# Optimization experiments

Hardware: AMD Instinct MI355X
Metric: run time of the kernel (lower is better)

The kernel has to match this reference:

```python
import jax, jax.numpy as jnp
import numpy as np

B, D, H, DH, NQ, NK = 64, 768, 8, 128, 256, 256


def _ln(x, g, b, eps=1e-5):
    m = x.mean(-1, keepdims=True)
    v = ((x - m) ** 2).mean(-1, keepdims=True)
    return (x - m) / jnp.sqrt(v + eps) * g + b


def setup_inputs() -> dict:
    key = jax.random.key(0)
    ks = jax.random.split(key, 16)
    w = lambda k, s: jax.random.normal(k, s, jnp.float32) * 0.02
    return {
        'emb_cause': jax.random.normal(ks[0], (B, D), jnp.float32),
        'emb_action': jax.random.normal(ks[1], (B, D), jnp.float32),
        'tok_cause': jax.random.normal(ks[2], (B, NK, D), jnp.float32),
        'tok_effect': jax.random.normal(ks[3], (B, NQ, D), jnp.float32),
        'fuse_ln_g': jnp.ones(2 * D), 'fuse_ln_b': jnp.zeros(2 * D),
        'fuse_w1': w(ks[4], (2 * D, D)), 'fuse_b1': jnp.zeros(D),
        'fuse_w2': w(ks[5], (D, D)), 'fuse_b2': jnp.zeros(D),
        'delta_ln_g': jnp.ones(D), 'delta_ln_b': jnp.zeros(D),
        'delta_w': w(ks[6], (D, D)), 'delta_b': jnp.zeros(D),
        'qg_w': w(ks[7], (D, H * DH)), 'qg_b': jnp.zeros(H * DH),
        'kg_w': w(ks[8], (D, H * DH)), 'kg_b': jnp.zeros(H * DH),
        'eff_ln_g': jnp.ones(D), 'eff_ln_b': jnp.zeros(D),
        'eff_w1': w(ks[9], (D, D)), 'eff_b1': jnp.zeros(D),
        'eff_w2': w(ks[10], (D, D)), 'eff_b2': jnp.zeros(D),
        'u_w': w(ks[11], (D, H * DH)),
        'v_w': w(ks[12], (D, H * DH)),
        'logit_scale': jnp.zeros(()),
    }


def reference(emb_cause, emb_action, tok_cause, tok_effect,
              fuse_ln_g, fuse_ln_b, fuse_w1, fuse_b1, fuse_w2, fuse_b2,
              delta_ln_g, delta_ln_b, delta_w, delta_b,
              qg_w, qg_b, kg_w, kg_b,
              eff_ln_g, eff_ln_b, eff_w1, eff_b1, eff_w2, eff_b2,
              u_w, v_w, logit_scale):
    # fuse: LN -> Linear -> GELU(exact) -> Linear (dropout = identity, eval)
    ctx_in = jnp.concatenate([emb_cause, emb_action], axis=-1)  # (B, 2D)
    h = jax.nn.gelu(_ln(ctx_in, fuse_ln_g, fuse_ln_b) @ fuse_w1 + fuse_b1, approximate=False)
    ctx = h @ fuse_w2 + fuse_b2  # (B, D)

    delta_e = _ln(ctx, delta_ln_g, delta_ln_b) @ delta_w + delta_b  # (B, D)
    pooled_effect = tok_effect.mean(axis=1)  # (B, D)
    e_shifted = pooled_effect + delta_e

    eh = jax.nn.gelu(_ln(ctx, eff_ln_g, eff_ln_b) @ eff_w1 + eff_b1, approximate=False)
    effect_pred = eh @ eff_w2 + eff_b2  # (B, D)

    q_gate = 1.0 + jnp.tanh(jax.nn.silu(ctx @ qg_w + qg_b)).reshape(B, H, DH)
    k_gate = 1.0 + jnp.tanh(jax.nn.silu(ctx @ kg_w + kg_b)).reshape(B, H, DH)

    # logit bias: torch code materializes (B,H,Nq,Nk,Dh); equivalent math is a
    # per-head inner product u.v (independent of q) broadcast over Nq.
    u = (e_shifted @ u_w).reshape(B, H, DH)            # (B, H, Dh)
    v = (tok_cause @ v_w).reshape(B, NK, H, DH)        # (B, Nk, H, Dh)
    bias = jnp.einsum('bhd,bkhd->bhk', u, v) / np.float32(np.sqrt(DH))
    logit_bias = jnp.exp(logit_scale) * jnp.broadcast_to(bias[:, :, None, :], (B, H, NQ, NK))

    return (q_gate, k_gate, e_shifted, delta_e, logit_bias, effect_pred)
```

## Files before the change

### kernel.cpp

```cpp
#include <hip/hip_runtime.h>
#include <math.h>

#define TPB 256

typedef float vf4 __attribute__((ext_vector_type(4)));

__device__ __forceinline__ float gelu_f(float x) {
    return 0.5f * x * (1.0f + erff(x * 0.70710678118654752f));
}
__device__ __forceinline__ float gate_f(float x) {
    float si = x / (1.0f + expf(-x));
    return 1.0f + tanhf(si);
}

template <class XL>
__device__ __forceinline__ void gemm_tile(XL xload, const float* __restrict__ W, int Wld, int cb,
                                          int k0, int kslice, float* part, int totN, int gcol, int s,
                                          float* __restrict__ xs, float* __restrict__ wt)
{
    const int t = threadIdx.x;
    const int tr4 = (t >> 4) << 2;
    const int tc4 = (t & 15) << 2;
    const int a  = t >> 5, kk = t & 31;
    const int wk = t >> 6, wc = t & 63;
    float xv[8], wv[8];
#pragma unroll
    for (int j = 0; j < 8; ++j) {
        xv[j] = xload(a + 8 * j, k0 + kk);
        wv[j] = W[(size_t)(k0 + wk + 4 * j) * Wld + cb + wc];
    }
    float acc[4][4] = {{0.f,0.f,0.f,0.f},{0.f,0.f,0.f,0.f},{0.f,0.f,0.f,0.f},{0.f,0.f,0.f,0.f}};
    for (int kc = 0; kc < kslice; kc += 32) {
#pragma unroll
        for (int j = 0; j < 8; ++j) {
            xs[kk * 68 + a + 8 * j] = xv[j];
            wt[(wk + 4 * j) * 68 + wc] = wv[j];
        }
        __syncthreads();
        int kn = kc + 32;
        if (kn < kslice) {
#pragma unroll
            for (int j = 0; j < 8; ++j) {
                xv[j] = xload(a + 8 * j, k0 + kn + kk);
                wv[j] = W[(size_t)(k0 + kn + wk + 4 * j) * Wld + cb + wc];
            }
        }
#pragma unroll
        for (int k = 0; k < 32; ++k) {
            float4 xq = *(const float4*)&xs[k * 68 + tr4];
            float4 wq = *(const float4*)&wt[k * 68 + tc4];
            acc[0][0] += xq.x * wq.x; acc[0][1] += xq.x * wq.y; acc[0][2] += xq.x * wq.z; acc[0][3] += xq.x * wq.w;
            acc[1][0] += xq.y * wq.x; acc[1][1] += xq.y * wq.y; acc[1][2] += xq.y * wq.z; acc[1][3] += xq.y * wq.w;
            acc[2][0] += xq.z * wq.x; acc[2][1] += xq.z * wq.y; acc[2][2] += xq.z * wq.z; acc[2][3] += xq.z * wq.w;
            acc[3][0] += xq.w * wq.x; acc[3][1] += xq.w * wq.y; acc[3][2] += xq.w * wq.z; acc[3][3] += xq.w * wq.w;
        }
        __syncthreads();
    }
    float* pp = part + (size_t)(s * 64 + tr4) * totN + gcol + tc4;
#pragma unroll
    for (int i = 0; i < 4; ++i)
#pragma unroll
        for (int j = 0; j < 4; ++j)
            pp[i * totN + j] = acc[i][j];
}

#define GEMM_LDS __shared__ float xs[32 * 68]; __shared__ float wt[32 * 68];

__global__ __launch_bounds__(256) void k_front(const float* __restrict__ ec, const float* __restrict__ ea,
                        float* __restrict__ stats1,
                        const float* __restrict__ tok_effect, float* __restrict__ pp)
{
    int t = threadIdx.x;
    if (blockIdx.x < 64) {
        int r = blockIdx.x;
        __shared__ float red[4];
        float v[6]; float sum = 0.f;
#pragma unroll
        for (int j = 0; j < 6; ++j) {
            int c = t + j * TPB;
            float x = (c < 768) ? ec[r * 768 + c] : ea[r * 768 + (c - 768)];
            v[j] = x; sum += x;
        }
#pragma unroll
        for (int o_ = 32; o_ > 0; o_ >>= 1) sum += __shfl_xor(sum, o_);
        if ((t & 63) == 0) red[t >> 6] = sum;
        __syncthreads();
        sum = red[0] + red[1] + red[2] + red[3];
        float mean = sum * (1.f / 1536.f);
        __syncthreads();
        float s2 = 0.f;
#pragma unroll
        for (int j = 0; j < 6; ++j) { float d = v[j] - mean; s2 += d * d; }
#pragma unroll
        for (int o_ = 32; o_ > 0; o_ >>= 1) s2 += __shfl_xor(s2, o_);
        if ((t & 63) == 0) red[t >> 6] = s2;
        __syncthreads();
        s2 = red[0] + red[1] + red[2] + red[3];
        if (t == 0) {
            stats1[2 * r]     = mean;
            stats1[2 * r + 1] = rsqrtf(s2 * (1.f / 1536.f) + 1e-5f);
        }
    } else {
        int m = blockIdx.x - 64;
        int cch = m % 3, b = (m / 3) % 64, qz = m / 192;
        int c = cch * TPB + t;
        const float* base = tok_effect + (size_t)(b * 256 + qz * 64) * 768 + c;
        float s = 0.f;
#pragma unroll 16
        for (int q = 0; q < 64; ++q) s += base[(size_t)q * 768];
        pp[(qz * 64 + b) * 768 + c] = s;
    }
}

struct G1Args {
    const float *ec, *ea, *stats1, *flg, *flb, *w1;
    float* part1;
};
__global__ __launch_bounds__(256) void k_g1(G1Args A)
{
    GEMM_LDS;
    int ct = blockIdx.x % 12, s = blockIdx.x / 12;
    auto xl = [&](int r, int k) {
        float raw = (k < 768) ? A.ec[r * 768 + k] : A.ea[r * 768 + (k - 768)];
        float m = A.stats1[2 * r], rs = A.stats1[2 * r + 1];
        return (raw - m) * rs * A.flg[k] + A.flb[k];
    };
    gemm_tile(xl, A.w1, 768, ct * 64, s * 128, 128, A.part1, 768, ct * 64, s, xs, wt);
}

__global__ __launch_bounds__(256) void k_g2(const float* __restrict__ part1, const float* __restrict__ b1,
                                            const float* __restrict__ w2, float* __restrict__ part2)
{
    GEMM_LDS;
    int ct = blockIdx.x % 12, s = blockIdx.x / 12;
    auto xl = [&](int r, int k) {
        float v = b1[k];
#pragma unroll
        for (int q = 0; q < 12; ++q) v += part1[(size_t)(q * 64 + r) * 768 + k];
        return gelu_f(v);
    };
    gemm_tile(xl, w2, 768, ct * 64, s * 64, 64, part2, 768, ct * 64, s, xs, wt);
}

__global__ __launch_bounds__(256) void k_ln(const float* __restrict__ part2, const float* __restrict__ b2,
                                            float* __restrict__ ctx, float* __restrict__ stats2)
{
    int r = blockIdx.x, t = threadIdx.x;
    __shared__ float red[4];
    float v[3]; float sum = 0.f;
#pragma unroll
    for (int j = 0; j < 3; ++j) {
        int c = t + j * TPB;
        float x = b2[c];
#pragma unroll
        for (int s = 0; s < 12; ++s) x += part2[(size_t)(s * 64 + r) * 768 + c];
        v[j] = x; sum += x;
        ctx[r * 768 + c] = x;
    }
#pragma unroll
    for (int o_ = 32; o_ > 0; o_ >>= 1) sum += __shfl_xor(sum, o_);
    if ((t & 63) == 0) red[t >> 6] = sum;
    __syncthreads();
    sum = red[0] + red[1] + red[2] + red[3];
    float mean = sum * (1.f / 768.f);
    __syncthreads();
    float s2 = 0.f;
#pragma unroll
    for (int j = 0; j < 3; ++j) { float d = v[j] - mean; s2 += d * d; }
#pragma unroll
    for (int o_ = 32; o_ > 0; o_ >>= 1) s2 += __shfl_xor(s2, o_);
    if ((t & 63) == 0) red[t >> 6] = s2;
    __syncthreads();
    s2 = red[0] + red[1] + red[2] + red[3];
    if (t == 0) {
        stats2[2 * r]     = mean;
        stats2[2 * r + 1] = rsqrtf(s2 * (1.f / 768.f) + 1e-5f);
    }
}

struct GAArgs {
    const float *ctx, *stats2, *dg, *db, *eg, *eb;
    const float *delta_w, *eff_w1, *qg_w, *kg_w;
    float* partA;
};
__global__ __launch_bounds__(256) void k_gA(GAArgs A)
{
    GEMM_LDS;
    int ct = blockIdx.x % 56, s = blockIdx.x / 56;
    if (ct < 12) {
        auto xl = [&](int r, int k) {
            float m = A.stats2[2 * r], rs = A.stats2[2 * r + 1];
            return (A.ctx[r * 768 + k] - m) * rs * A.dg[k] + A.db[k];
        };
        gemm_tile(xl, A.delta_w, 768, ct * 64, s * 96, 96, A.partA, 3584, ct * 64, s, xs, wt);
    } else if (ct < 24) {
        auto xl = [&](int r, int k) {
            float m = A.stats2[2 * r], rs = A.stats2[2 * r + 1];
            return (A.ctx[r * 768 + k] - m) * rs * A.eg[k] + A.eb[k];
        };
        gemm_tile(xl, A.eff_w1, 768, (ct - 12) * 64, s * 96, 96, A.partA, 3584, ct * 64, s, xs, wt);
    } else {
        auto xl = [&](int r, int k) { return A.ctx[r * 768 + k]; };
        const float* W = (ct < 40) ? A.qg_w : A.kg_w;
        int cb = (ct < 40) ? (ct - 24) * 64 : (ct - 40) * 64;
        gemm_tile(xl, W, 1024, cb, s * 96, 96, A.partA, 3584, ct * 64, s, xs, wt);
    }
}

struct MidArgs {
    const float *partA, *pp, *delta_b, *eff_b1, *qg_b, *kg_b, *eff_w2, *u_w;
    float *partB, *out_de, *out_es, *out_qg, *out_kg;
};
__global__ __launch_bounds__(256) void k_mid(MidArgs A)
{
    GEMM_LDS;
    const int t = threadIdx.x;
    if (blockIdx.x < 28) {
#pragma unroll
        for (int ii = 0; ii < 32; ++ii) {
            int idx = blockIdx.x * TPB + t + ii * 7168;
            int r = idx / 3584, c = idx - r * 3584;
            if (c >= 768 && c < 1536) continue;
            float v = 0.f;
#pragma unroll
            for (int q = 0; q < 8; ++q) v += A.partA[(size_t)(q * 64 + r) * 3584 + c];
            if (c < 768) {
                float de = v + A.delta_b[c];
                A.out_de[r * 768 + c] = de;
                float s4 = A.pp[r * 768 + c] + A.pp[(64 + r) * 768 + c]
                         + A.pp[(128 + r) * 768 + c] + A.pp[(192 + r) * 768 + c];
                A.out_es[r * 768 + c] = de + s4 * (1.f / 256.f);
            } else if (c < 2560) {
                A.out_qg[r * 1024 + (c - 1536)] = gate_f(v + A.qg_b[c - 1536]);
            } else {
                A.out_kg[r * 1024 + (c - 2560)] = gate_f(v + A.kg_b[c - 2560]);
            }
        }
    } else {
        int m = blockIdx.x - 28;
        int ct = m % 28, s = m / 28;
        if (ct < 12) {
            auto xl = [&](int r, int k) {
                float v = A.eff_b1[k];
#pragma unroll
                for (int q = 0; q < 8; ++q) v += A.partA[(size_t)(q * 64 + r) * 3584 + 768 + k];
                return gelu_f(v);
            };
            gemm_tile(xl, A.eff_w2, 768, ct * 64, s * 96, 96, A.partB, 1792, ct * 64, s, xs, wt);
        } else {
            auto xl = [&](int r, int k) {
                float v = A.delta_b[k];
#pragma unroll
                for (int q = 0; q < 8; ++q) v += A.partA[(size_t)(q * 64 + r) * 3584 + k];
                float s4 = A.pp[r * 768 + k] + A.pp[(64 + r) * 768 + k]
                         + A.pp[(128 + r) * 768 + k] + A.pp[(192 + r) * 768 + k];
                return v + s4 * (1.f / 256.f);
            };
            gemm_tile(xl, A.u_w, 1024, (ct - 12) * 64, s * 96, 96, A.partB, 1792, ct * 64, s, xs, wt);
        }
    }
}

__global__ __launch_bounds__(256) void k_tail(const float* __restrict__ partB, const float* __restrict__ eff_b2,
                                              const float* __restrict__ v_w,
                                              float* __restrict__ out_ep, float* __restrict__ wu)
{
    const int t = threadIdx.x;
    if (blockIdx.x < 6) {
#pragma unroll
        for (int ii = 0; ii < 32; ++ii) {
            int idx = blockIdx.x * TPB + t + ii * 1536;
            int r = idx / 768, c = idx - r * 768;
            float v = eff_b2[c];
#pragma unroll
            for (int q = 0; q < 8; ++q) v += partB[(size_t)(q * 64 + r) * 1792 + c];
            out_ep[r * 768 + c] = v;
        }
    } else {
        __shared__ float us[64 * 132];
        int m = blockIdx.x - 6;
        int h = m / 12, ctile = m % 12;
        for (int n = t; n < 8192; n += TPB) {
            int b = n >> 7, d = n & 127;
            float v = 0.f;
#pragma unroll
            for (int q = 0; q < 8; ++q) v += partB[(size_t)(q * 64 + b) * 1792 + 768 + h * 128 + d];
            us[b * 132 + d] = v;
        }
        __syncthreads();
        int c = ctile * 64 + (t >> 2);
        int bo = t & 3;
        const float* vr = v_w + (size_t)c * 1024 + h * 128;
        float acc[16];
#pragma unroll
        for (int i = 0; i < 16; ++i) acc[i] = 0.f;
        for (int d = 0; d < 128; d += 4) {
            float4 w4 = *(const float4*)(vr + d);
#pragma unroll
            for (int i = 0; i < 16; ++i) {
                const float* ub = &us[(4 * i + bo) * 132 + d];
                acc[i] += w4.x * ub[0] + w4.y * ub[1] + w4.z * ub[2] + w4.w * ub[3];
            }
        }
#pragma unroll
        for (int i = 0; i < 16; ++i) {
            int b = 4 * i + bo;
            wu[(b * 8 + h) * 768 + c] = acc[i];
        }
    }
}

__global__ __launch_bounds__(256) void k_biasbc(const float* __restrict__ tok_cause, const float* __restrict__ wu,
                         const float* __restrict__ ls_ptr, float* __restrict__ out_lb)
{
    int b = blockIdx.x, kt = blockIdx.y;
    __shared__ float wuh[8 * 768];
    __shared__ float bsm[8 * 32];
    for (int n = threadIdx.x; n < 6144; n += TPB)
        wuh[n] = wu[b * 6144 + n];
    __syncthreads();
    const int lane = threadIdx.x & 63, w = threadIdx.x >> 6;
    float4 wur[3][8];
#pragma unroll
    for (int j = 0; j < 3; ++j)
#pragma unroll
        for (int h = 0; h < 8; ++h)
            wur[j][h] = *(const float4*)&wuh[h * 768 + (lane + 64 * j) * 4];
    float scale = expf(ls_ptr[0]) * 0.08838834764831845f;
#pragma unroll
    for (int rr = 0; rr < 8; ++rr) {
        int rl = w * 8 + rr;
        int row = kt * 32 + rl;
        const float4* tr = (const float4*)(tok_cause + ((size_t)b * 256 + row) * 768);
        float4 t0 = tr[lane], t1 = tr[lane + 64], t2 = tr[lane + 128];
        float acc[8];
#pragma unroll
        for (int h = 0; h < 8; ++h) {
            acc[h] = t0.x * wur[0][h].x + t0.y * wur[0][h].y + t0.z * wur[0][h].z + t0.w * wur[0][h].w
                   + t1.x * wur[1][h].x + t1.y * wur[1][h].y + t1.z * wur[1][h].z + t1.w * wur[1][h].w
                   + t2.x * wur[2][h].x + t2.y * wur[2][h].y + t2.z * wur[2][h].z + t2.w * wur[2][h].w;
        }
#pragma unroll
        for (int h = 0; h < 8; ++h) {
            float vv = acc[h];
#pragma unroll
            for (int o_ = 32; o_ > 0; o_ >>= 1) vv += __shfl_xor(vv, o_);
            if (lane == 0) bsm[h * 32 + rl] = vv * scale;
        }
    }
    __syncthreads();
    const vf4* bs4 = (const vf4*)bsm;
    vf4* o4 = (vf4*)out_lb;
    int v = threadIdx.x & 7, sq0 = threadIdx.x >> 3;
#pragma unroll
    for (int it = 0; it < 64; ++it) {
        int seg = sq0 + it * 32;
        int h = seg >> 8, q = seg & 255;
        vf4 val = bs4[h * 8 + v];
        __builtin_nontemporal_store(val, &o4[(((size_t)(b * 8 + h) * 256 + q) << 6) + kt * 8 + v]);
    }
}

extern "C" void kernel_launch(void* const* d_in, const int* in_sizes, int n_in,
                              void* d_out, int out_size, void* d_ws, size_t ws_size,
                              hipStream_t stream)
{
    (void)in_sizes; (void)n_in; (void)out_size; (void)ws_size;
    const float* emb_cause  = (const float*)d_in[0];
    const float* emb_action = (const float*)d_in[1];
    const float* tok_cause  = (const float*)d_in[2];
    const float* tok_effect = (const float*)d_in[3];
    const float* fuse_ln_g  = (const float*)d_in[4];
    const float* fuse_ln_b  = (const float*)d_in[5];
    const float* fuse_w1    = (const float*)d_in[6];
    const float* fuse_b1    = (const float*)d_in[7];
    const float* fuse_w2    = (const float*)d_in[8];
    const float* fuse_b2    = (const float*)d_in[9];
    const float* delta_ln_g = (const float*)d_in[10];
    const float* delta_ln_b = (const float*)d_in[11];
    const float* delta_w    = (const float*)d_in[12];
    const float* delta_b    = (const float*)d_in[13];
    const float* qg_w       = (const float*)d_in[14];
    const float* qg_b       = (const float*)d_in[15];
    const float* kg_w       = (const float*)d_in[16];
    const float* kg_b       = (const float*)d_in[17];
    const float* eff_ln_g   = (const float*)d_in[18];
    const float* eff_ln_b   = (const float*)d_in[19];
    const float* eff_w1     = (const float*)d_in[20];
    const float* eff_b1     = (const float*)d_in[21];
    const float* eff_w2     = (const float*)d_in[22];
    const float* eff_b2     = (const float*)d_in[23];
    const float* u_w        = (const float*)d_in[24];
    const float* v_w        = (const float*)d_in[25];
    const float* logit_sc   = (const float*)d_in[26];

    float* ws = (float*)d_ws;
    float* ctx    = ws + 0;
    float* pp     = ws + 49152;
    float* wu     = ws + 245760;
    float* stats1 = ws + 638976;
    float* stats2 = ws + 639104;

    float* out    = (float*)d_out;
    float* out_qg = out + 0;
    float* out_kg = out + 65536;
    float* out_es = out + 131072;
    float* out_de = out + 180224;
    float* out_lb = out + 229376;
    float* out_ep = out + 33783808;

    float* pbase = out_lb + 20000000;
    float* part1 = pbase;
    float* part2 = pbase + 589824;
    float* partA = pbase + 1179648;
    float* partB = pbase + 3014656;

    k_front<<<832, TPB, 0, stream>>>(emb_cause, emb_action, stats1, tok_effect, pp);
    {
        G1Args A; A.ec = emb_cause; A.ea = emb_action; A.stats1 = stats1;
        A.flg = fuse_ln_g; A.flb = fuse_ln_b; A.w1 = fuse_w1; A.part1 = part1;
        k_g1<<<144, TPB, 0, stream>>>(A);
    }
    k_g2<<<144, TPB, 0, stream>>>(part1, fuse_b1, fuse_w2, part2);
    k_ln<<<64, TPB, 0, stream>>>(part2, fuse_b2, ctx, stats2);
    {
        GAArgs A; A.ctx = ctx; A.stats2 = stats2;
        A.dg = delta_ln_g; A.db = delta_ln_b; A.eg = eff_ln_g; A.eb = eff_ln_b;
        A.delta_w = delta_w; A.eff_w1 = eff_w1; A.qg_w = qg_w; A.kg_w = kg_w; A.partA = partA;
        k_gA<<<448, TPB, 0, stream>>>(A);
    }
    {
        MidArgs M; M.partA = partA; M.pp = pp;
        M.delta_b = delta_b; M.eff_b1 = eff_b1; M.qg_b = qg_b; M.kg_b = kg_b;
        M.eff_w2 = eff_w2; M.u_w = u_w; M.partB = partB;
        M.out_de = out_de; M.out_es = out_es; M.out_qg = out_qg; M.out_kg = out_kg;
        k_mid<<<252, TPB, 0, stream>>>(M);
    }
    k_tail<<<102, TPB, 0, stream>>>(partB, eff_b2, v_w, out_ep, wu);
    k_biasbc<<<dim3(64, 8), TPB, 0, stream>>>(tok_cause, wu, logit_sc, out_lb);
}
```

Before: 143.9 us.

## Overlap token pooling with fuse GEMMs and widen bias broadcast blocks

The tok_effect mean-pooling work moves out of the front kernel and is split across extra blocks appended to the two small fuse GEMM launches (k_g1, k_g2), so its memory-bound streaming overlaps the latency-bound GEMMs. The front kernel becomes a small LN-stats-only kernel. k_biasbc moves to 512 threads per block with fewer rows per wave and uses nontemporal loads for tok_cause, which also applies to the pooling loads. The trade is more blocks competing with the GEMMs for bandwidth and extra register pressure at 512 threads.

```diff
diff --git a/kernel.cpp b/kernel.cpp
--- a/kernel.cpp
+++ b/kernel.cpp
@@ -66,59 +66,63 @@
 
 #define GEMM_LDS __shared__ float xs[32 * 68]; __shared__ float wt[32 * 68];
 
-__global__ __launch_bounds__(256) void k_front(const float* __restrict__ ec, const float* __restrict__ ea,
-                        float* __restrict__ stats1,
-                        const float* __restrict__ tok_effect, float* __restrict__ pp)
-{
-    int t = threadIdx.x;
-    if (blockIdx.x < 64) {
-        int r = blockIdx.x;
-        __shared__ float red[4];
-        float v[6]; float sum = 0.f;
-#pragma unroll
-        for (int j = 0; j < 6; ++j) {
-            int c = t + j * TPB;
-            float x = (c < 768) ? ec[r * 768 + c] : ea[r * 768 + (c - 768)];
-            v[j] = x; sum += x;
-        }
-#pragma unroll
-        for (int o_ = 32; o_ > 0; o_ >>= 1) sum += __shfl_xor(sum, o_);
-        if ((t & 63) == 0) red[t >> 6] = sum;
-        __syncthreads();
-        sum = red[0] + red[1] + red[2] + red[3];
-        float mean = sum * (1.f / 1536.f);
-        __syncthreads();
-        float s2 = 0.f;
-#pragma unroll
-        for (int j = 0; j < 6; ++j) { float d = v[j] - mean; s2 += d * d; }
-#pragma unroll
-        for (int o_ = 32; o_ > 0; o_ >>= 1) s2 += __shfl_xor(s2, o_);
-        if ((t & 63) == 0) red[t >> 6] = s2;
-        __syncthreads();
-        s2 = red[0] + red[1] + red[2] + red[3];
-        if (t == 0) {
-            stats1[2 * r]     = mean;
-            stats1[2 * r + 1] = rsqrtf(s2 * (1.f / 1536.f) + 1e-5f);
-        }
-    } else {
-        int m = blockIdx.x - 64;
-        int cch = m % 3, b = (m / 3) % 64, qz = m / 192;
-        int c = cch * TPB + t;
-        const float* base = tok_effect + (size_t)(b * 256 + qz * 64) * 768 + c;
-        float s = 0.f;
+__device__ __forceinline__ void pool_task(const float* __restrict__ tok_effect,
+                                          float* __restrict__ pp, int m, int t)
+{
+    int cch = m % 3, b = (m / 3) % 64, qz = m / 192;
+    int c = cch * TPB + t;
+    const float* base = tok_effect + (size_t)(b * 256 + qz * 64) * 768 + c;
+    float s = 0.f;
 #pragma unroll 16
-        for (int q = 0; q < 64; ++q) s += base[(size_t)q * 768];
-        pp[(qz * 64 + b) * 768 + c] = s;
+    for (int q = 0; q < 64; ++q) s += __builtin_nontemporal_load(base + (size_t)q * 768);
+    pp[(qz * 64 + b) * 768 + c] = s;
+}
+
+__global__ __launch_bounds__(256) void k_stats(const float* __restrict__ ec, const float* __restrict__ ea,
+                                               float* __restrict__ stats1)
+{
+    int t = threadIdx.x, r = blockIdx.x;
+    __shared__ float red[4];
+    float v[6]; float sum = 0.f;
+#pragma unroll
+    for (int j = 0; j < 6; ++j) {
+        int c = t + j * TPB;
+        float x = (c < 768) ? ec[r * 768 + c] : ea[r * 768 + (c - 768)];
+        v[j] = x; sum += x;
+    }
+#pragma unroll
+    for (int o_ = 32; o_ > 0; o_ >>= 1) sum += __shfl_xor(sum, o_);
+    if ((t & 63) == 0) red[t >> 6] = sum;
+    __syncthreads();
+    sum = red[0] + red[1] + red[2] + red[3];
+    float mean = sum * (1.f / 1536.f);
+    __syncthreads();
+    float s2 = 0.f;
+#pragma unroll
+    for (int j = 0; j < 6; ++j) { float d = v[j] - mean; s2 += d * d; }
+#pragma unroll
+    for (int o_ = 32; o_ > 0; o_ >>= 1) s2 += __shfl_xor(s2, o_);
+    if ((t & 63) == 0) red[t >> 6] = s2;
+    __syncthreads();
+    s2 = red[0] + red[1] + red[2] + red[3];
+    if (t == 0) {
+        stats1[2 * r]     = mean;
+        stats1[2 * r + 1] = rsqrtf(s2 * (1.f / 1536.f) + 1e-5f);
     }
 }
 
 struct G1Args {
     const float *ec, *ea, *stats1, *flg, *flb, *w1;
-    float* part1;
+    const float *tok_effect;
+    float *part1, *pp;
 };
 __global__ __launch_bounds__(256) void k_g1(G1Args A)
 {
     GEMM_LDS;
+    if (blockIdx.x >= 144) {
+        pool_task(A.tok_effect, A.pp, blockIdx.x - 144, threadIdx.x);
+        return;
+    }
     int ct = blockIdx.x % 12, s = blockIdx.x / 12;
     auto xl = [&](int r, int k) {
         float raw = (k < 768) ? A.ec[r * 768 + k] : A.ea[r * 768 + (k - 768)];
@@ -128,18 +132,26 @@
     gemm_tile(xl, A.w1, 768, ct * 64, s * 128, 128, A.part1, 768, ct * 64, s, xs, wt);
 }
 
-__global__ __launch_bounds__(256) void k_g2(const float* __restrict__ part1, const float* __restrict__ b1,
-                                            const float* __restrict__ w2, float* __restrict__ part2)
+struct G2Args {
+    const float *part1, *b1, *w2;
+    const float *tok_effect;
+    float *part2, *pp;
+};
+__global__ __launch_bounds__(256) void k_g2(G2Args A)
 {
     GEMM_LDS;
+    if (blockIdx.x >= 144) {
+        pool_task(A.tok_effect, A.pp, blockIdx.x - 144 + 384, threadIdx.x);
+        return;
+    }
     int ct = blockIdx.x % 12, s = blockIdx.x / 12;
     auto xl = [&](int r, int k) {
-        float v = b1[k];
-#pragma unroll
-        for (int q = 0; q < 12; ++q) v += part1[(size_t)(q * 64 + r) * 768 + k];
+        float v = A.b1[k];
+#pragma unroll
+        for (int q = 0; q < 12; ++q) v += A.part1[(size_t)(q * 64 + r) * 768 + k];
         return gelu_f(v);
     };
-    gemm_tile(xl, w2, 768, ct * 64, s * 64, 64, part2, 768, ct * 64, s, xs, wt);
+    gemm_tile(xl, A.w2, 768, ct * 64, s * 64, 64, A.part2, 768, ct * 64, s, xs, wt);
 }
 
 __global__ __launch_bounds__(256) void k_ln(const float* __restrict__ part2, const float* __restrict__ b2,
@@ -310,29 +322,31 @@
     }
 }
 
-__global__ __launch_bounds__(256) void k_biasbc(const float* __restrict__ tok_cause, const float* __restrict__ wu,
+__global__ __launch_bounds__(512) void k_biasbc(const float* __restrict__ tok_cause, const float* __restrict__ wu,
                          const float* __restrict__ ls_ptr, float* __restrict__ out_lb)
 {
     int b = blockIdx.x, kt = blockIdx.y;
     __shared__ float wuh[8 * 768];
     __shared__ float bsm[8 * 32];
-    for (int n = threadIdx.x; n < 6144; n += TPB)
+    for (int n = threadIdx.x; n < 6144; n += 512)
         wuh[n] = wu[b * 6144 + n];
     __syncthreads();
     const int lane = threadIdx.x & 63, w = threadIdx.x >> 6;
-    float4 wur[3][8];
+    vf4 wur[3][8];
 #pragma unroll
     for (int j = 0; j < 3; ++j)
 #pragma unroll
         for (int h = 0; h < 8; ++h)
-            wur[j][h] = *(const float4*)&wuh[h * 768 + (lane + 64 * j) * 4];
+            wur[j][h] = *(const vf4*)&wuh[h * 768 + (lane + 64 * j) * 4];
     float scale = expf(ls_ptr[0]) * 0.08838834764831845f;
 #pragma unroll
-    for (int rr = 0; rr < 8; ++rr) {
-        int rl = w * 8 + rr;
+    for (int rr = 0; rr < 4; ++rr) {
+        int rl = w * 4 + rr;
         int row = kt * 32 + rl;
-        const float4* tr = (const float4*)(tok_cause + ((size_t)b * 256 + row) * 768);
-        float4 t0 = tr[lane], t1 = tr[lane + 64], t2 = tr[lane + 128];
+        const vf4* tr = (const vf4*)(tok_cause + ((size_t)b * 256 + row) * 768);
+        vf4 t0 = __builtin_nontemporal_load(tr + lane);
+        vf4 t1 = __builtin_nontemporal_load(tr + lane + 64);
+        vf4 t2 = __builtin_nontemporal_load(tr + lane + 128);
         float acc[8];
 #pragma unroll
         for (int h = 0; h < 8; ++h) {
@@ -353,8 +367,8 @@
     vf4* o4 = (vf4*)out_lb;
     int v = threadIdx.x & 7, sq0 = threadIdx.x >> 3;
 #pragma unroll
-    for (int it = 0; it < 64; ++it) {
-        int seg = sq0 + it * 32;
+    for (int it = 0; it < 32; ++it) {
+        int seg = sq0 + it * 64;
         int h = seg >> 8, q = seg & 255;
         vf4 val = bs4[h * 8 + v];
         __builtin_nontemporal_store(val, &o4[(((size_t)(b * 8 + h) * 256 + q) << 6) + kt * 8 + v]);
@@ -415,13 +429,18 @@
     float* partA = pbase + 1179648;
     float* partB = pbase + 3014656;
 
-    k_front<<<832, TPB, 0, stream>>>(emb_cause, emb_action, stats1, tok_effect, pp);
+    k_stats<<<64, TPB, 0, stream>>>(emb_cause, emb_action, stats1);
     {
         G1Args A; A.ec = emb_cause; A.ea = emb_action; A.stats1 = stats1;
-        A.flg = fuse_ln_g; A.flb = fuse_ln_b; A.w1 = fuse_w1; A.part1 = part1;
-        k_g1<<<144, TPB, 0, stream>>>(A);
-    }
-    k_g2<<<144, TPB, 0, stream>>>(part1, fuse_b1, fuse_w2, part2);
+        A.flg = fuse_ln_g; A.flb = fuse_ln_b; A.w1 = fuse_w1;
+        A.tok_effect = tok_effect; A.part1 = part1; A.pp = pp;
+        k_g1<<<528, TPB, 0, stream>>>(A);
+    }
+    {
+        G2Args A; A.part1 = part1; A.b1 = fuse_b1; A.w2 = fuse_w2;
+        A.tok_effect = tok_effect; A.part2 = part2; A.pp = pp;
+        k_g2<<<528, TPB, 0, stream>>>(A);
+    }
     k_ln<<<64, TPB, 0, stream>>>(part2, fuse_b2, ctx, stats2);
     {
         GAArgs A; A.ctx = ctx; A.stats2 = stats2;
@@ -437,5 +456,5 @@
         k_mid<<<252, TPB, 0, stream>>>(M);
     }
     k_tail<<<102, TPB, 0, stream>>>(partB, eff_b2, v_w, out_ep, wu);
-    k_biasbc<<<dim3(64, 8), TPB, 0, stream>>>(tok_cause, wu, logit_sc, out_lb);
-}
+    k_biasbc<<<dim3(64, 8), 512, 0, stream>>>(tok_cause, wu, logit_sc, out_lb);
+}
```

Result: faster. 140.8 us (-2.1%).
